# Kernel optimization log

Hardware: AMD Instinct MI355X
Metric: run time of the kernel (lower is better)

## Reference

```python
import jax, jax.numpy as jnp
import numpy as np

NUM_CLASSES = 5
TEMPERATURE = 3.0
BATCH = 4_194_304


def setup_inputs() -> dict:
    key = jax.random.key(0)
    k1, k2 = jax.random.split(key)
    quality_score = jax.random.uniform(k1, (BATCH,), dtype=jnp.float32)
    class_logits = jax.random.normal(k2, (BATCH, NUM_CLASSES), dtype=jnp.float32)
    return {"quality_score": quality_score, "class_logits": class_logits}


def _soft_targets(score, num_classes):
    # Vectorized version of the per-sample python loop in the torch module.
    C = num_classes
    # int(clamp(score*C, 0, C-1)) -> floor for non-negative scores
    idx = jnp.floor(jnp.clip(score * C, 0.0, C - 1)).astype(jnp.int32)
    center = (idx.astype(score.dtype) + 0.5) / C
    dist = jnp.abs(score - center) * C
    cond_lo = (idx > 0) & (score < center)          # spill to class idx-1
    cond_hi = (idx < C - 1) & (score > center)      # spill to class idx+1
    has_nb = cond_lo | cond_hi
    main_val = jnp.where(has_nb, 1.0 - dist, 1.0)
    nb_idx = idx - cond_lo.astype(jnp.int32) + cond_hi.astype(jnp.int32)
    nb_val = jnp.where(has_nb, dist, 0.0)
    cols = jnp.arange(C)
    # [B, C] dense soft targets built by broadcasted one-hot masks (no scatter)
    soft = (main_val[:, None] * (cols[None, :] == idx[:, None])
            + nb_val[:, None] * (cols[None, :] == nb_idx[:, None]))
    return soft


def reference(quality_score, class_logits):
    T = TEMPERATURE
    C = class_logits.shape[-1]
    B = class_logits.shape[0]
    soft = _soft_targets(quality_score, C)
    p = jax.nn.softmax(soft / T, axis=-1)               # targets (probs)
    logq = jax.nn.log_softmax(class_logits / T, axis=-1)
    # F.kl_div(logq, p, reduction='batchmean') = sum p*(log p - logq) / B
    kl = jnp.sum(p * (jnp.log(p) - logq)) / B
    return kl * T * T
```

## Files before the change

### kernel.cpp

```cpp
#include <hip/hip_runtime.h>
#include <math.h>


constexpr int   kC     = 5;
constexpr float kInvT  = 1.0f / 3.0f;
constexpr int   kBatch = 4194304;

__global__ void zero_out_kernel(float* out) {
    if (threadIdx.x == 0) out[0] = 0.0f;
}

__global__ __launch_bounds__(256) void kl_partial_kernel(
    const float* __restrict__ score,
    const float* __restrict__ logits,
    float* __restrict__ out,
    int nquads ) {

    float acc = 0.0f;
    const int stride = gridDim.x * blockDim.x;

    for (int q = blockIdx.x * blockDim.x + threadIdx.x; q < nquads; q += stride) {
        const float4 s4 = reinterpret_cast<const float4*>(score)[q];
        const float4* lrow = reinterpret_cast<const float4*>(logits + (size_t)q * 20);
        const float4 L0 = lrow[0], L1 = lrow[1], L2 = lrow[2], L3 = lrow[3], L4 = lrow[4];

        const float v[20] = {L0.x, L0.y, L0.z, L0.w,
                             L1.x, L1.y, L1.z, L1.w,
                             L2.x, L2.y, L2.z, L2.w,
                             L3.x, L3.y, L3.z, L3.w,
                             L4.x, L4.y, L4.z, L4.w};
        const float ss[4] = {s4.x, s4.y, s4.z, s4.w};

        #pragma unroll
        for (int r = 0; r < 4; ++r) {
            const float s = ss[r];

            float sc = fminf(fmaxf(s * 5.0f, 0.0f), 4.0f);
            int idx = (int)sc;
            float center = ((float)idx + 0.5f) * 0.2f;
            float dist = fabsf(s - center) * 5.0f;
            bool lo = (idx > 0) && (s < center);
            bool hi = (idx < kC - 1) && (s > center);
            bool nb = lo || hi;
            float mv = nb ? (1.0f - dist) : 1.0f;
            float nv = nb ? dist : 0.0f;
            int nbi = idx + (hi ? 1 : 0) - (lo ? 1 : 0);

            float m = v[r * 5 + 0];
            #pragma unroll
            for (int c = 1; c < kC; ++c) m = fmaxf(m, v[r * 5 + c]);

            float Zq = 0.0f, Zp = 0.0f, Spa = 0.0f, Spl = 0.0f;
            #pragma unroll
            for (int c = 0; c < kC; ++c) {
                const float l = v[r * 5 + c];
                Zq += expf((l - m) * kInvT);
                const float a = (c == idx ? mv : 0.0f) + (c == nbi ? nv : 0.0f);
                const float e = expf(a * kInvT);
                Zp += e;
                Spa += e * a;
                Spl += e * l;
            }
            acc += kInvT * ((Spa - Spl) / Zp + m) - logf(Zp) + logf(Zq);
        }
    }

    #pragma unroll
    for (int off = 32; off > 0; off >>= 1) acc += __shfl_down(acc, off, 64);

    __shared__ float wsum[4];
    const int lane = threadIdx.x & 63;
    const int wave = threadIdx.x >> 6;
    if (lane == 0) wsum[wave] = acc;
    __syncthreads();
    if (threadIdx.x == 0) {
        const float b = wsum[0] + wsum[1] + wsum[2] + wsum[3];
        atomicAdd(out, b * (9.0f / (float)kBatch));
    }
}

extern "C" void kernel_launch(void* const* d_in, const int* in_sizes, int n_in,
                              void* d_out, int out_size, void* d_ws, size_t ws_size,
                              hipStream_t stream) {
    const float* score  = (const float*)d_in[0];
    const float* logits = (const float*)d_in[1];
    float* out = (float*)d_out;

    const int B = in_sizes[0];
    const int nquads = B / 4;

    zero_out_kernel<<<1, 64, 0, stream>>>(out);
    kl_partial_kernel<<<1024, 256, 0, stream>>>(score, logits, out, nquads);
}
```

Before: 142.1 us.

## Exploit two-nonzero soft targets and use fast exp/log intrinsics in KL kernel

Each row's target softmax is rewritten in closed form: only the main and neighbour classes have nonzero soft targets, so the other three contribute exp(0)=1 each. This cuts the per-row target exponentials from five to two and replaces the per-class selects with direct picks of the two logits. The max-subtraction for the logit log-sum-exp is dropped, and expf/logf/division become __expf, __logf and a hardware reciprocal. The aim is to cut transcendental and ALU work in a kernel that appears compute-bound. The cost is lower precision and possible overflow for very large logits.

```diff
diff --git a/kernel.cpp b/kernel.cpp
--- a/kernel.cpp
+++ b/kernel.cpp
@@ -33,35 +33,39 @@
 
         #pragma unroll
         for (int r = 0; r < 4; ++r) {
-            const float s = ss[r];
+            const float s  = ss[r];
+            const float l0 = v[r * 5 + 0], l1 = v[r * 5 + 1], l2 = v[r * 5 + 2],
+                        l3 = v[r * 5 + 3], l4 = v[r * 5 + 4];
 
-            float sc = fminf(fmaxf(s * 5.0f, 0.0f), 4.0f);
-            int idx = (int)sc;
-            float center = ((float)idx + 0.5f) * 0.2f;
-            float dist = fabsf(s - center) * 5.0f;
-            bool lo = (idx > 0) && (s < center);
-            bool hi = (idx < kC - 1) && (s > center);
-            bool nb = lo || hi;
-            float mv = nb ? (1.0f - dist) : 1.0f;
-            float nv = nb ? dist : 0.0f;
-            int nbi = idx + (hi ? 1 : 0) - (lo ? 1 : 0);
+            const float sc     = fminf(fmaxf(s * 5.0f, 0.0f), 4.0f);
+            const int   idx    = (int)sc;
+            const float center = ((float)idx + 0.5f) * 0.2f;
+            float       d      = fabsf(s - center) * 5.0f;
+            const bool  lo     = (idx > 0) && (s < center);
+            const bool  hi     = (idx < kC - 1) && (s > center);
+            const bool  nb     = lo || hi;
+            d = nb ? d : 0.0f;
+            const int nbi = idx + (hi ? 1 : 0) - (lo ? 1 : 0);
 
-            float m = v[r * 5 + 0];
-            #pragma unroll
-            for (int c = 1; c < kC; ++c) m = fmaxf(m, v[r * 5 + c]);
+            const float e_main = __expf((1.0f - d) * kInvT);
+            const float e_nb   = __expf(d * kInvT);
 
-            float Zq = 0.0f, Zp = 0.0f, Spa = 0.0f, Spl = 0.0f;
-            #pragma unroll
-            for (int c = 0; c < kC; ++c) {
-                const float l = v[r * 5 + c];
-                Zq += expf((l - m) * kInvT);
-                const float a = (c == idx ? mv : 0.0f) + (c == nbi ? nv : 0.0f);
-                const float e = expf(a * kInvT);
-                Zp += e;
-                Spa += e * a;
-                Spl += e * l;
-            }
-            acc += kInvT * ((Spa - Spl) / Zp + m) - logf(Zp) + logf(Zq);
+            const float S = l0 + l1 + l2 + l3 + l4;
+            const float l_main = (idx == 0) ? l0 : (idx == 1) ? l1 :
+                                 (idx == 2) ? l2 : (idx == 3) ? l3 : l4;
+            const float l_nb   = (nbi == 0) ? l0 : (nbi == 1) ? l1 :
+                                 (nbi == 2) ? l2 : (nbi == 3) ? l3 : l4;
+
+            const float Zq = __expf(l0 * kInvT) + __expf(l1 * kInvT) +
+                             __expf(l2 * kInvT) + __expf(l3 * kInvT) +
+                             __expf(l4 * kInvT);
+
+            const float Zp  = e_main + e_nb + 3.0f;
+            const float Spa = e_main * (1.0f - d) + e_nb * d;
+            const float Spl = e_main * l_main + e_nb * l_nb + (S - l_main - l_nb);
+
+            acc += kInvT * (Spa - Spl) * __builtin_amdgcn_rcpf(Zp)
+                   - __logf(Zp) + __logf(Zq);
         }
     }
 
```

After: 140.2 us. Within noise of the previous version (-1.3%).
